# Performance work log

Measured on AMD Instinct MI355X. Metric: run time of the kernel, lower is better.

The kernel has to match this reference:

```python
import jax, jax.numpy as jnp
import numpy as np

HIDDEN = 32  # hard-coded in EdgeModel's Sequential

def setup_inputs() -> dict:
    key = jax.random.key(0)
    ks = jax.random.split(key, 9)
    E, FN, FE, OUT = 200000, 512, 256, 128
    IN = FN + FN + FE  # 1280
    src = jax.random.normal(ks[0], (E, FN), dtype=jnp.float32)
    dest = jax.random.normal(ks[1], (E, FN), dtype=jnp.float32)
    edge_attr = jax.random.normal(ks[2], (E, FE), dtype=jnp.float32)
    u = jax.random.normal(ks[3], (64, 128), dtype=jnp.float32)
    batch = jax.random.randint(ks[4], (E,), 0, 64, dtype=jnp.int64)
    # Linear params, PyTorch default init scale ~ 1/sqrt(fan_in)
    s1 = 1.0 / np.sqrt(IN)
    s2 = 1.0 / np.sqrt(HIDDEN)
    W1 = jax.random.uniform(ks[5], (IN, HIDDEN), jnp.float32, -s1, s1)
    b1 = jax.random.uniform(ks[6], (HIDDEN,), jnp.float32, -s1, s1)
    W2 = jax.random.uniform(ks[7], (HIDDEN, OUT), jnp.float32, -s2, s2)
    b2 = jax.random.uniform(ks[8], (OUT,), jnp.float32, -s2, s2)
    return {"src": src, "dest": dest, "edge_attr": edge_attr, "u": u,
            "batch": batch, "W1": W1, "b1": b1, "W2": W2, "b2": b2}

def reference(src, dest, edge_attr, u, batch, W1, b1, W2, b2):
    # concat along feature dim, then Linear -> ELU -> Linear (u, batch unused)
    x = jnp.concatenate([src, dest, edge_attr], axis=1)  # [E, 2*FN+FE]
    h = jax.nn.elu(x @ W1 + b1)                           # [E, 32]
    return h @ W2 + b2                                    # [E, OUT]
```

## Files before the change

kernel.cpp:

```cpp
#include <hip/hip_runtime.h>
#include <hip/hip_bf16.h>

typedef __bf16 bf16x8 __attribute__((ext_vector_type(8)));
typedef unsigned short u16x8 __attribute__((ext_vector_type(8)));
typedef float f32x4 __attribute__((ext_vector_type(4)));

using gptr_t = const __attribute__((address_space(1))) unsigned int*;
using lptr_t = __attribute__((address_space(3))) unsigned int*;
#define gp(x) ((gptr_t)(const void*)(x))
#define lp(x) ((lptr_t)(void*)(x))

__global__ __launch_bounds__(256) void prep_w_kernel(
    const float* __restrict__ W1, const float* __restrict__ W2,
    unsigned short* __restrict__ wsB1, unsigned short* __restrict__ wsB2) {
  int tid = blockIdx.x * 256 + threadIdx.x;
  if (tid < 40960) {
    int j = tid & 7, l = (tid >> 3) & 63, nt = (tid >> 9) & 1, kt = tid >> 10;
    int k = kt * 32 + ((l >> 4) << 3) + j;
    int n = nt * 16 + (l & 15);
    __bf16 v = (__bf16)W1[k * 32 + n];
    wsB1[tid] = __builtin_bit_cast(unsigned short, v);
  } else if (tid < 45056) {
    int t = tid - 40960;
    int j = t & 7, l = (t >> 3) & 63, nt = t >> 9;
    int k = ((l >> 4) << 3) + j;
    int n = nt * 16 + (l & 15);
    __bf16 v = (__bf16)W2[k * 128 + n];
    wsB2[t] = __builtin_bit_cast(unsigned short, v);
  }
}

template <bool USE_WS>
__global__ __launch_bounds__(256) void edge_mlp_kernel(
    const float* __restrict__ src, const float* __restrict__ dst,
    const float* __restrict__ ea, const float* __restrict__ W1,
    const float* __restrict__ b1, const float* __restrict__ W2,
    const float* __restrict__ b2, const unsigned short* __restrict__ wsB1,
    const unsigned short* __restrict__ wsB2, float* __restrict__ out, int nE) {
  __shared__ alignas(16) float xb[2][64][64];
  const int lane = threadIdx.x & 63;
  const int wave = threadIdx.x >> 6;
  const int l15 = lane & 15;
  const int lh = lane >> 4;

  const int nwg = gridDim.x;
  const int q = nwg >> 3, rmd = nwg & 7;
  const int xcd = (int)blockIdx.x & 7, idx = (int)blockIdx.x >> 3;
  const int bid =
      (xcd < rmd ? xcd * (q + 1) : rmd * (q + 1) + (xcd - rmd) * q) + idx;

  const long e0 = (long)bid * 64;
  if (e0 >= nE) return;
  const long erow = e0 + wave * 16 + l15;

  const float bias0 = b1[l15];
  const float bias1 = b1[16 + l15];

  f32x4 acc0 = {0.f, 0.f, 0.f, 0.f};
  f32x4 acc1 = {0.f, 0.f, 0.f, 0.f};

  if constexpr (USE_WS) {
    auto stage = [&](int c, int b) {
#pragma unroll
      for (int r = 0; r < 4; ++r) {
        const int row_l = r * 16 + wave * 4 + (lane >> 4);
        const int i = lane & 15;
        const int g = ((((i >> 1) ^ (row_l & 7)) << 1) | (i & 1));
        const float* p;
        if (c < 8)
          p = src + (e0 + row_l) * 512 + c * 64 + g * 4;
        else if (c < 16)
          p = dst + (e0 + row_l) * 512 + (c - 8) * 64 + g * 4;
        else
          p = ea + (e0 + row_l) * 256 + (c - 16) * 64 + g * 4;
        __builtin_amdgcn_global_load_lds(
            gp(p), lp(&xb[b][r * 16 + wave * 4][0]), 16, 0, 0);
      }
    };

    auto consume = [&](int c, int b) {
      const int lr = wave * 16 + l15;
#pragma unroll
      for (int kk = 0; kk < 2; ++kk) {
        const int pp = (kk * 4 + lh) ^ (lr & 7);
        const f32x4* ap =
            (const f32x4*)((const char*)&xb[b][lr][0] + pp * 32);
        f32x4 lo = ap[0], hi = ap[1];
        bf16x8 a;
        a[0] = (__bf16)lo[0]; a[1] = (__bf16)lo[1];
        a[2] = (__bf16)lo[2]; a[3] = (__bf16)lo[3];
        a[4] = (__bf16)hi[0]; a[5] = (__bf16)hi[1];
        a[6] = (__bf16)hi[2]; a[7] = (__bf16)hi[3];
        const int t = c * 2 + kk;
        bf16x8 b0 = __builtin_bit_cast(
            bf16x8, *(const u16x8*)(wsB1 + (t * 2 + 0) * 512 + lane * 8));
        bf16x8 b1f = __builtin_bit_cast(
            bf16x8, *(const u16x8*)(wsB1 + (t * 2 + 1) * 512 + lane * 8));
        acc0 = __builtin_amdgcn_mfma_f32_16x16x32_bf16(a, b0, acc0, 0, 0, 0);
        acc1 = __builtin_amdgcn_mfma_f32_16x16x32_bf16(a, b1f, acc1, 0, 0, 0);
      }
    };

    stage(0, 0);
    __syncthreads();
#pragma unroll
    for (int c = 0; c < 20; ++c) {
      if (c < 19) stage(c + 1, (c + 1) & 1);
      consume(c, c & 1);
      if (c < 19) __syncthreads();
    }
  } else {
    long rowf = erow < nE ? erow : nE - 1;
    for (int t = 0; t < 40; ++t) {
      const float* p = (t < 16) ? (src + rowf * 512 + t * 32 + lh * 8)
                     : (t < 32) ? (dst + rowf * 512 + (t - 16) * 32 + lh * 8)
                                : (ea + rowf * 256 + (t - 32) * 32 + lh * 8);
      f32x4 lo = *(const f32x4*)p;
      f32x4 hi = *(const f32x4*)(p + 4);
      bf16x8 a, bf0, bf1;
      a[0] = (__bf16)lo[0]; a[1] = (__bf16)lo[1];
      a[2] = (__bf16)lo[2]; a[3] = (__bf16)lo[3];
      a[4] = (__bf16)hi[0]; a[5] = (__bf16)hi[1];
      a[6] = (__bf16)hi[2]; a[7] = (__bf16)hi[3];
#pragma unroll
      for (int j = 0; j < 8; ++j) {
        int k = t * 32 + lh * 8 + j;
        bf0[j] = (__bf16)W1[k * 32 + l15];
        bf1[j] = (__bf16)W1[k * 32 + 16 + l15];
      }
      acc0 = __builtin_amdgcn_mfma_f32_16x16x32_bf16(a, bf0, acc0, 0, 0, 0);
      acc1 = __builtin_amdgcn_mfma_f32_16x16x32_bf16(a, bf1, acc1, 0, 0, 0);
    }
  }

  unsigned short* hl = ((unsigned short*)&xb[0][0][0]) + wave * 2048;
#pragma unroll
  for (int r = 0; r < 4; ++r) {
    int hrow = lh * 4 + r;
    float h0 = acc0[r] + bias0;
    float h1 = acc1[r] + bias1;
    h0 = h0 > 0.f ? h0 : (__expf(h0) - 1.f);
    h1 = h1 > 0.f ? h1 : (__expf(h1) - 1.f);
    __bf16 v0 = (__bf16)h0, v1 = (__bf16)h1;
    hl[hrow * 40 + l15] = __builtin_bit_cast(unsigned short, v0);
    hl[hrow * 40 + 16 + l15] = __builtin_bit_cast(unsigned short, v1);
  }
  asm volatile("s_waitcnt lgkmcnt(0)" ::: "memory");
  __builtin_amdgcn_sched_barrier(0);
  bf16x8 ha =
      __builtin_bit_cast(bf16x8, *(const u16x8*)(hl + l15 * 40 + lh * 8));

  f32x4 o[8];
#pragma unroll
  for (int nt = 0; nt < 8; ++nt) {
    bf16x8 bw;
    if (USE_WS) {
      bw = __builtin_bit_cast(bf16x8,
                              *(const u16x8*)(wsB2 + nt * 512 + lane * 8));
    } else {
#pragma unroll
      for (int j = 0; j < 8; ++j)
        bw[j] = (__bf16)W2[(lh * 8 + j) * 128 + nt * 16 + l15];
    }
    f32x4 z = {0.f, 0.f, 0.f, 0.f};
    o[nt] = __builtin_amdgcn_mfma_f32_16x16x32_bf16(ha, bw, z, 0, 0, 0);
  }

  const long ebase = e0 + wave * 16;
#pragma unroll
  for (int nt = 0; nt < 8; ++nt) {
    float bb = b2[nt * 16 + l15];
#pragma unroll
    for (int r = 0; r < 4; ++r) {
      long e = ebase + lh * 4 + r;
      if (e < nE) out[e * 128 + nt * 16 + l15] = o[nt][r] + bb;
    }
  }
}

extern "C" void kernel_launch(void* const* d_in, const int* in_sizes, int n_in,
                              void* d_out, int out_size, void* d_ws,
                              size_t ws_size, hipStream_t stream) {
  const float* src = (const float*)d_in[0];
  const float* dst = (const float*)d_in[1];
  const float* ea = (const float*)d_in[2];
  const float* W1 = (const float*)d_in[5];
  const float* b1 = (const float*)d_in[6];
  const float* W2 = (const float*)d_in[7];
  const float* b2 = (const float*)d_in[8];
  float* out = (float*)d_out;

  const int nE = in_sizes[0] / 512;

  unsigned short* wsB1 = (unsigned short*)d_ws;
  unsigned short* wsB2 = wsB1 + 40960;
  const bool use_ws =
      ws_size >= 45056 * sizeof(unsigned short) && (nE & 63) == 0;

  if (use_ws) {
    const int nblocks = nE / 64;
    prep_w_kernel<<<176, 256, 0, stream>>>(W1, W2, wsB1, wsB2);
    edge_mlp_kernel<true><<<nblocks, 256, 0, stream>>>(
        src, dst, ea, W1, b1, W2, b2, wsB1, wsB2, out, nE);
  } else {
    const long strips = (nE + 15) / 16;
    const int nblocks = (int)((strips + 3) / 4);
    edge_mlp_kernel<false><<<nblocks, 256, 0, stream>>>(
        src, dst, ea, W1, b1, W2, b2, nullptr, nullptr, out, nE);
  }
}
```

Before: 244.5 us.

## Triple-buffer per-wave row strips with vmcnt waits instead of double-buffer sync

```diff
diff --git a/kernel.cpp b/kernel.cpp
--- a/kernel.cpp
+++ b/kernel.cpp
@@ -9,6 +9,13 @@
 using lptr_t = __attribute__((address_space(3))) unsigned int*;
 #define gp(x) ((gptr_t)(const void*)(x))
 #define lp(x) ((lptr_t)(void*)(x))
+
+#define VMW(N)                                            \
+  do {                                                    \
+    asm volatile("s_waitcnt vmcnt(" #N ")" ::: "memory"); \
+    __builtin_amdgcn_sched_barrier(0);                    \
+  } while (0)
+#define MEMFENCE asm volatile("" ::: "memory")
 
 __global__ __launch_bounds__(256) void prep_w_kernel(
     const float* __restrict__ W1, const float* __restrict__ W2,
@@ -37,7 +44,7 @@
     const float* __restrict__ b1, const float* __restrict__ W2,
     const float* __restrict__ b2, const unsigned short* __restrict__ wsB1,
     const unsigned short* __restrict__ wsB2, float* __restrict__ out, int nE) {
-  __shared__ alignas(16) float xb[2][64][64];
+  __shared__ alignas(16) float xb[3][16][256];
   const int lane = threadIdx.x & 63;
   const int wave = threadIdx.x >> 6;
   const int l15 = lane & 15;
@@ -51,7 +58,6 @@
 
   const long e0 = (long)bid * 64;
   if (e0 >= nE) return;
-  const long erow = e0 + wave * 16 + l15;
 
   const float bias0 = b1[l15];
   const float bias1 = b1[16 + l15];
@@ -60,57 +66,68 @@
   f32x4 acc1 = {0.f, 0.f, 0.f, 0.f};
 
   if constexpr (USE_WS) {
-    auto stage = [&](int c, int b) {
-#pragma unroll
-      for (int r = 0; r < 4; ++r) {
-        const int row_l = r * 16 + wave * 4 + (lane >> 4);
-        const int i = lane & 15;
-        const int g = ((((i >> 1) ^ (row_l & 7)) << 1) | (i & 1));
+    auto stage = [&](int c, int s) {
+#pragma unroll
+      for (int i = 0; i < 4; ++i) {
+        const int r = wave * 4 + i;
+        const int unit = ((((lane >> 1) ^ (r & 7)) << 1) | (lane & 1));
         const float* p;
-        if (c < 8)
-          p = src + (e0 + row_l) * 512 + c * 64 + g * 4;
-        else if (c < 16)
-          p = dst + (e0 + row_l) * 512 + (c - 8) * 64 + g * 4;
-        else
-          p = ea + (e0 + row_l) * 256 + (c - 16) * 64 + g * 4;
-        __builtin_amdgcn_global_load_lds(
-            gp(p), lp(&xb[b][r * 16 + wave * 4][0]), 16, 0, 0);
+        if (c < 8) {
+          const int sw = c >> 1, h = c & 1;
+          p = src + (e0 + sw * 16 + r) * 512 + h * 256 + unit * 4;
+        } else if (c < 16) {
+          const int sw = (c - 8) >> 1, h = c & 1;
+          p = dst + (e0 + sw * 16 + r) * 512 + h * 256 + unit * 4;
+        } else {
+          const int sw = c - 16;
+          p = ea + (e0 + sw * 16 + r) * 256 + unit * 4;
+        }
+        __builtin_amdgcn_global_load_lds(gp(p), lp(&xb[s][r][0]), 16, 0, 0);
       }
     };
 
-    auto consume = [&](int c, int b) {
-      const int lr = wave * 16 + l15;
-#pragma unroll
-      for (int kk = 0; kk < 2; ++kk) {
-        const int pp = (kk * 4 + lh) ^ (lr & 7);
+    auto consume = [&](int c, int s) {
+      const int tbase = (c < 8) ? (c & 1) * 8
+                      : (c < 16) ? 16 + (c & 1) * 8
+                                 : 32;
+#pragma unroll
+      for (int tt = 0; tt < 8; ++tt) {
+        const int pp = (tt * 4 + lh) ^ (l15 & 7);
         const f32x4* ap =
-            (const f32x4*)((const char*)&xb[b][lr][0] + pp * 32);
+            (const f32x4*)((const char*)&xb[s][l15][0] + pp * 32);
         f32x4 lo = ap[0], hi = ap[1];
         bf16x8 a;
         a[0] = (__bf16)lo[0]; a[1] = (__bf16)lo[1];
         a[2] = (__bf16)lo[2]; a[3] = (__bf16)lo[3];
         a[4] = (__bf16)hi[0]; a[5] = (__bf16)hi[1];
         a[6] = (__bf16)hi[2]; a[7] = (__bf16)hi[3];
-        const int t = c * 2 + kk;
-        bf16x8 b0 = __builtin_bit_cast(
+        const int t = tbase + tt;
+        bf16x8 w0 = __builtin_bit_cast(
             bf16x8, *(const u16x8*)(wsB1 + (t * 2 + 0) * 512 + lane * 8));
-        bf16x8 b1f = __builtin_bit_cast(
+        bf16x8 w1 = __builtin_bit_cast(
             bf16x8, *(const u16x8*)(wsB1 + (t * 2 + 1) * 512 + lane * 8));
-        acc0 = __builtin_amdgcn_mfma_f32_16x16x32_bf16(a, b0, acc0, 0, 0, 0);
-        acc1 = __builtin_amdgcn_mfma_f32_16x16x32_bf16(a, b1f, acc1, 0, 0, 0);
+        acc0 = __builtin_amdgcn_mfma_f32_16x16x32_bf16(a, w0, acc0, 0, 0, 0);
+        acc1 = __builtin_amdgcn_mfma_f32_16x16x32_bf16(a, w1, acc1, 0, 0, 0);
       }
     };
 
     stage(0, 0);
-    __syncthreads();
+    stage(1, 1);
+    stage(2, 2);
 #pragma unroll
     for (int c = 0; c < 20; ++c) {
-      if (c < 19) stage(c + 1, (c + 1) & 1);
-      consume(c, c & 1);
-      if (c < 19) __syncthreads();
+      if (c <= 17) { VMW(8); } else if (c == 18) { VMW(4); } else { VMW(0); }
+      __builtin_amdgcn_s_barrier();
+      MEMFENCE;
+      const int wc = (c < 8) ? (c >> 1) : (c < 16) ? ((c - 8) >> 1) : (c - 16);
+      if (wave == wc) consume(c, c % 3);
+      MEMFENCE;
+      __builtin_amdgcn_s_barrier();
+      if (c + 3 < 20) stage(c + 3, (c + 3) % 3);
     }
   } else {
-    long rowf = erow < nE ? erow : nE - 1;
+    long rowf = e0 + wave * 16 + l15;
+    if (rowf >= nE) rowf = nE - 1;
     for (int t = 0; t < 40; ++t) {
       const float* p = (t < 16) ? (src + rowf * 512 + t * 32 + lh * 8)
                      : (t < 32) ? (dst + rowf * 512 + (t - 16) * 32 + lh * 8)
```

After: 295.9 us. 1.21x slower.

## Triple-buffer LDS staging and prefetch weight fragments with buffer loads

Applied to the files above, without the earlier changes.

```diff
diff --git a/kernel.cpp b/kernel.cpp
--- a/kernel.cpp
+++ b/kernel.cpp
@@ -4,11 +4,19 @@
 typedef __bf16 bf16x8 __attribute__((ext_vector_type(8)));
 typedef unsigned short u16x8 __attribute__((ext_vector_type(8)));
 typedef float f32x4 __attribute__((ext_vector_type(4)));
+typedef unsigned int u32x4 __attribute__((ext_vector_type(4)));
 
 using gptr_t = const __attribute__((address_space(1))) unsigned int*;
 using lptr_t = __attribute__((address_space(3))) unsigned int*;
 #define gp(x) ((gptr_t)(const void*)(x))
 #define lp(x) ((lptr_t)(void*)(x))
+
+#define VMW(N)                                            \
+  do {                                                    \
+    asm volatile("s_waitcnt vmcnt(" #N ")" ::: "memory"); \
+    __builtin_amdgcn_sched_barrier(0);                    \
+  } while (0)
+#define MEMFENCE asm volatile("" ::: "memory")
 
 __global__ __launch_bounds__(256) void prep_w_kernel(
     const float* __restrict__ W1, const float* __restrict__ W2,
@@ -30,6 +38,25 @@
   }
 }
 
+__device__ __forceinline__ u32x4 make_srd(const void* p, unsigned bytes) {
+  u32x4 r;
+  r[0] = (unsigned)(unsigned long long)p;
+  r[1] = (unsigned)(((unsigned long long)p) >> 32);
+  r[2] = bytes;
+  r[3] = 0x00020000u;
+  return r;
+}
+
+#define WLD(BUF, SOFF)                                                      \
+  asm volatile("buffer_load_dwordx4 %0, %4, %5, %6 offen offset:0\n\t"      \
+               "buffer_load_dwordx4 %1, %4, %5, %6 offen offset:1024\n\t"   \
+               "buffer_load_dwordx4 %2, %4, %5, %6 offen offset:2048\n\t"   \
+               "buffer_load_dwordx4 %3, %4, %5, %6 offen offset:3072"       \
+               : "=&v"(pw[BUF][0]), "=&v"(pw[BUF][1]), "=&v"(pw[BUF][2]),   \
+                 "=&v"(pw[BUF][3])                                          \
+               : "v"(voffw), "s"(srdw), "s"((unsigned)(SOFF))               \
+               : "memory")
+
 template <bool USE_WS>
 __global__ __launch_bounds__(256) void edge_mlp_kernel(
     const float* __restrict__ src, const float* __restrict__ dst,
@@ -37,7 +64,7 @@
     const float* __restrict__ b1, const float* __restrict__ W2,
     const float* __restrict__ b2, const unsigned short* __restrict__ wsB1,
     const unsigned short* __restrict__ wsB2, float* __restrict__ out, int nE) {
-  __shared__ alignas(16) float xb[2][64][64];
+  __shared__ alignas(16) float xb[3][64][64];
   const int lane = threadIdx.x & 63;
   const int wave = threadIdx.x >> 6;
   const int l15 = lane & 15;
@@ -51,7 +78,6 @@
 
   const long e0 = (long)bid * 64;
   if (e0 >= nE) return;
-  const long erow = e0 + wave * 16 + l15;
 
   const float bias0 = b1[l15];
   const float bias1 = b1[16 + l15];
@@ -60,12 +86,15 @@
   f32x4 acc1 = {0.f, 0.f, 0.f, 0.f};
 
   if constexpr (USE_WS) {
-    auto stage = [&](int c, int b) {
+    const u32x4 srdw = make_srd(wsB1, 81920u);
+    const unsigned voffw = (unsigned)lane * 16u;
+    u16x8 pw[3][4];
+
+    auto stage = [&](int c, int s) {
 #pragma unroll
       for (int r = 0; r < 4; ++r) {
-        const int row_l = r * 16 + wave * 4 + (lane >> 4);
-        const int i = lane & 15;
-        const int g = ((((i >> 1) ^ (row_l & 7)) << 1) | (i & 1));
+        const int row_l = r * 16 + wave * 4 + lh;
+        const int g = ((((l15 >> 1) ^ (row_l & 7)) << 1) | (l15 & 1));
         const float* p;
         if (c < 8)
           p = src + (e0 + row_l) * 512 + c * 64 + g * 4;
@@ -74,43 +103,53 @@
         else
           p = ea + (e0 + row_l) * 256 + (c - 16) * 64 + g * 4;
         __builtin_amdgcn_global_load_lds(
-            gp(p), lp(&xb[b][r * 16 + wave * 4][0]), 16, 0, 0);
+            gp(p), lp(&xb[s][r * 16 + wave * 4][0]), 16, 0, 0);
       }
     };
 
-    auto consume = [&](int c, int b) {
+    auto consume = [&](int c, int s) {
       const int lr = wave * 16 + l15;
 #pragma unroll
       for (int kk = 0; kk < 2; ++kk) {
         const int pp = (kk * 4 + lh) ^ (lr & 7);
         const f32x4* ap =
-            (const f32x4*)((const char*)&xb[b][lr][0] + pp * 32);
+            (const f32x4*)((const char*)&xb[s][lr][0] + pp * 32);
         f32x4 lo = ap[0], hi = ap[1];
         bf16x8 a;
         a[0] = (__bf16)lo[0]; a[1] = (__bf16)lo[1];
         a[2] = (__bf16)lo[2]; a[3] = (__bf16)lo[3];
         a[4] = (__bf16)hi[0]; a[5] = (__bf16)hi[1];
         a[6] = (__bf16)hi[2]; a[7] = (__bf16)hi[3];
-        const int t = c * 2 + kk;
-        bf16x8 b0 = __builtin_bit_cast(
-            bf16x8, *(const u16x8*)(wsB1 + (t * 2 + 0) * 512 + lane * 8));
-        bf16x8 b1f = __builtin_bit_cast(
-            bf16x8, *(const u16x8*)(wsB1 + (t * 2 + 1) * 512 + lane * 8));
-        acc0 = __builtin_amdgcn_mfma_f32_16x16x32_bf16(a, b0, acc0, 0, 0, 0);
-        acc1 = __builtin_amdgcn_mfma_f32_16x16x32_bf16(a, b1f, acc1, 0, 0, 0);
+        acc0 = __builtin_amdgcn_mfma_f32_16x16x32_bf16(
+            a, __builtin_bit_cast(bf16x8, pw[c % 3][kk * 2 + 0]), acc0, 0, 0, 0);
+        acc1 = __builtin_amdgcn_mfma_f32_16x16x32_bf16(
+            a, __builtin_bit_cast(bf16x8, pw[c % 3][kk * 2 + 1]), acc1, 0, 0, 0);
       }
     };
 
-    stage(0, 0);
-    __syncthreads();
+    stage(0, 0); WLD(0, 0);
+    stage(1, 1); WLD(1, 4096);
+
 #pragma unroll
     for (int c = 0; c < 20; ++c) {
-      if (c < 19) stage(c + 1, (c + 1) & 1);
-      consume(c, c & 1);
-      if (c < 19) __syncthreads();
+      if (c < 19) { VMW(8); } else { VMW(0); }
+      __builtin_amdgcn_s_barrier();
+      __builtin_amdgcn_sched_barrier(0);
+      MEMFENCE;
+      if (c + 2 < 20) {
+        stage(c + 2, (c + 2) % 3);
+        switch ((c + 2) % 3) {
+          case 0: WLD(0, (c + 2) * 4096); break;
+          case 1: WLD(1, (c + 2) * 4096); break;
+          default: WLD(2, (c + 2) * 4096); break;
+        }
+      }
+      consume(c, c % 3);
+      MEMFENCE;
     }
   } else {
-    long rowf = erow < nE ? erow : nE - 1;
+    long rowf = e0 + wave * 16 + l15;
+    if (rowf >= nE) rowf = nE - 1;
     for (int t = 0; t < 40; ++t) {
       const float* p = (t < 16) ? (src + rowf * 512 + t * 32 + lh * 8)
                      : (t < 32) ? (dst + rowf * 512 + (t - 16) * 32 + lh * 8)
```

New measurement: 249.5 us. 2.0% more time.
